# Optimization experiments

Measured on AMD Instinct MI355X. Metric: run time of the kernel, lower is better.

The kernel has to match this reference:

```python
import jax, jax.numpy as jnp
import numpy as np

N, E, IN_F, G, LATENT, HIDDEN, STEPS = 50000, 800000, 7, 16, 64, 128, 3
LN_EPS = 1e-6  # flax LayerNorm default


def setup_inputs() -> dict:
    key = jax.random.key(0)

    def rn(i, shape, scale=1.0):
        return jax.random.normal(jax.random.fold_in(key, i), shape, dtype=jnp.float32) * scale

    return {
        "nodes": rn(0, (N, IN_F)),
        "senders": jax.random.randint(jax.random.fold_in(key, 1), (E,), 0, N, dtype=jnp.int32),
        "receivers": jax.random.randint(jax.random.fold_in(key, 2), (E,), 0, N, dtype=jnp.int32),
        "g": rn(3, (G,)),
        "embed_w": rn(4, (IN_F, LATENT), IN_F ** -0.5),
        "embed_b": jnp.zeros((LATENT,), jnp.float32),
        "edge_w1_first": rn(5, (2 * LATENT + G, HIDDEN), (2 * LATENT + G) ** -0.5),
        "edge_w1_rest": rn(6, (STEPS - 1, 3 * LATENT + G, HIDDEN), (3 * LATENT + G) ** -0.5),
        "edge_b1": jnp.zeros((STEPS, HIDDEN), jnp.float32),
        "edge_w2": rn(7, (STEPS, HIDDEN, LATENT), HIDDEN ** -0.5),
        "edge_b2": jnp.zeros((STEPS, LATENT), jnp.float32),
        "node_w1": rn(8, (STEPS, 2 * LATENT + G, HIDDEN), (2 * LATENT + G) ** -0.5),
        "node_b1": jnp.zeros((STEPS, HIDDEN), jnp.float32),
        "node_w2": rn(9, (STEPS, HIDDEN, LATENT), HIDDEN ** -0.5),
        "node_b2": jnp.zeros((STEPS, LATENT), jnp.float32),
        "ln_scale": jnp.ones((STEPS, LATENT), jnp.float32),
        "ln_bias": jnp.zeros((STEPS, LATENT), jnp.float32),
        "dec_w": rn(10, (LATENT, IN_F), LATENT ** -0.5),
        "dec_b": jnp.zeros((IN_F,), jnp.float32),
    }


def _layer_norm(x, scale, bias):
    mu = jnp.mean(x, axis=-1, keepdims=True)
    var = jnp.var(x, axis=-1, keepdims=True)
    return (x - mu) * jax.lax.rsqrt(var + LN_EPS) * scale + bias


def reference(nodes, senders, receivers, g, embed_w, embed_b,
              edge_w1_first, edge_w1_rest, edge_b1, edge_w2, edge_b2,
              node_w1, node_b1, node_w2, node_b2, ln_scale, ln_bias,
              dec_w, dec_b):
    n_node = nodes.shape[0]
    n_edge = senders.shape[0]
    # node embedder (GraphMapFeatures with Dense(latent_size))
    h = nodes @ embed_w + embed_b                      # [N, LATENT]
    ge = jnp.broadcast_to(g[None, :], (n_edge, g.shape[0]))  # globals per edge
    gn = jnp.broadcast_to(g[None, :], (n_node, g.shape[0]))  # globals per node
    e = None
    for t in range(STEPS):
        s = h[senders]                                 # [E, LATENT] gather
        r = h[receivers]                               # [E, LATENT] gather
        if t == 0:
            # edges are None on the first step -> concat(senders, receivers, globals)
            e_in = jnp.concatenate([s, r, ge], axis=1)
            w1 = edge_w1_first
        else:
            e_in = jnp.concatenate([e, s, r, ge], axis=1)
            w1 = edge_w1_rest[t - 1]
        # edge MLP: Dense(hidden)+gelu, Dense(latent)
        e = jax.nn.gelu(e_in @ w1 + edge_b1[t]) @ edge_w2[t] + edge_b2[t]
        # aggregate messages at receivers (jraph default segment_sum)
        recv = jax.ops.segment_sum(e, receivers, num_segments=n_node)
        # node MLP on concat(nodes, received, globals)
        n_in = jnp.concatenate([h, recv, gn], axis=1)
        upd = jax.nn.gelu(n_in @ node_w1[t] + node_b1[t]) @ node_w2[t] + node_b2[t]
        h = h + upd                                    # skip connection on nodes
        h = _layer_norm(h, ln_scale[t], ln_bias[t])
    # node decoder back to in_features
    return h @ dec_w + dec_b
```

## Files before the change

kernel.cpp:

```cpp
#include <hip/hip_runtime.h>

#define NN 50000
#define NE 800000
#define INF 7
#define GD 16
#define LAT 64
#define HID 128

typedef unsigned short u16;
typedef __attribute__((ext_vector_type(8))) __bf16 bf16x8;
typedef __attribute__((ext_vector_type(4))) float f32x4;

__device__ __forceinline__ float bf2f(u16 u) {
  union { unsigned int i; float f; } v; v.i = ((unsigned int)u) << 16; return v.f;
}
__device__ __forceinline__ float blo(unsigned int u) {
  union { unsigned int i; float f; } v; v.i = u << 16; return v.f;
}
__device__ __forceinline__ float bhi(unsigned int u) {
  union { unsigned int i; float f; } v; v.i = u & 0xffff0000u; return v.f;
}
__device__ __forceinline__ u16 f2bf(float f) {
  union { float f; unsigned int i; } v; v.f = f;
  unsigned int x = v.i;
  return (u16)((x + 0x7fffu + ((x >> 16) & 1u)) >> 16);
}
__device__ __forceinline__ float gelu(float x) {
  float u = x * x;
  float p = fmaf(0.044715f * u, x, x);
  float e = __expf(-1.5957691216057308f * p);
  return x * __builtin_amdgcn_rcpf(e + 1.0f);
}

struct PackJobs {
  const float* src[13];
  u16* dst[13];
  int K[13];
  int N[13];
  int KC[13];
};

__global__ void pack_all(PackJobs J) {
  const int j = blockIdx.y;
  const int KC = J.KC[j];
  const float* W = J.src[j];
  u16* out = J.dst[j];
  int t = blockIdx.x * blockDim.x + threadIdx.x;
  if (KC == 0) {
    if (t < 32) out[t] = (t < GD) ? f2bf(W[t]) : (u16)0;
    return;
  }
  const int K = J.K[j], N = J.N[j];
  const int NT = N >> 4;
  if (t >= KC * NT * 64) return;
  int l = t & 63;
  int nt = (t >> 6) % NT;
  int kc = t / (64 * NT);
  int n = nt * 16 + (l & 15);
  int kbase = kc * 32 + (l >> 4) * 8;
  ushort4 lo, hi;
  u16 v[8];
#pragma unroll
  for (int jj = 0; jj < 8; ++jj) {
    int k = kbase + jj;
    v[jj] = (k < K) ? f2bf(W[k * N + n]) : (u16)0;
  }
  lo.x = v[0]; lo.y = v[1]; lo.z = v[2]; lo.w = v[3];
  hi.x = v[4]; hi.y = v[5]; hi.z = v[6]; hi.w = v[7];
  ushort4* dst = (ushort4*)&out[(size_t)t * 8];
  dst[0] = lo; dst[1] = hi;
}

__global__ void hist_kernel(const int* __restrict__ rcv, int* __restrict__ cnt) {
  int i = blockIdx.x * blockDim.x + threadIdx.x;
  if (i < NE) atomicAdd(&cnt[rcv[i]], 1);
}

__launch_bounds__(1024)
__global__ void scan_kernel(const int* __restrict__ cnt, int* __restrict__ rowptr,
                            int* __restrict__ cursor) {
  __shared__ int wsum[16];
  const int t = threadIdx.x;
  const int lane = t & 63;
  const int wid = t >> 6;
  int carry = 0;
  for (int base = 0; base < NN; base += 1024) {
    const int i = base + t;
    int v = (i < NN) ? cnt[i] : 0;
    int x = v;
#pragma unroll
    for (int off = 1; off < 64; off <<= 1) {
      int y = __shfl_up(x, off);
      if (lane >= off) x += y;
    }
    if (lane == 63) wsum[wid] = x;
    __syncthreads();
    if (wid == 0 && lane < 16) {
      int s = wsum[lane];
#pragma unroll
      for (int off = 1; off < 16; off <<= 1) {
        int y = __shfl_up(s, off);
        if (lane >= off) s += y;
      }
      wsum[lane] = s;
    }
    __syncthreads();
    const int excl = carry + (wid > 0 ? wsum[wid - 1] : 0) + (x - v);
    if (i < NN) { rowptr[i] = excl; cursor[i] = excl; }
    carry += wsum[15];
    __syncthreads();
  }
  if (t == 0) rowptr[NN] = NE;
}

__global__ void scatter_kernel(const int* __restrict__ snd, const int* __restrict__ rcv,
                               int* __restrict__ cursor, int* __restrict__ ssnd,
                               int* __restrict__ srcv) {
  int i = blockIdx.x * blockDim.x + threadIdx.x;
  if (i >= NE) return;
  int r = rcv[i];
  int p = atomicAdd(&cursor[r], 1);
  ssnd[p] = snd[i];
  srcv[p] = r;
}

__global__ void embed_kernel(const float* __restrict__ nodes, const float* __restrict__ w,
                             const float* __restrict__ b, float* __restrict__ h,
                             u16* __restrict__ hbf) {
  int gid = blockIdx.x * blockDim.x + threadIdx.x;
  if (gid >= NN * LAT) return;
  int n = gid >> 6, j = gid & 63;
  float acc = b[j];
#pragma unroll
  for (int k = 0; k < INF; ++k)
    acc = fmaf(nodes[n * INF + k], w[k * LAT + j], acc);
  h[gid] = acc;
  hbf[gid] = f2bf(acc);
}

__launch_bounds__(256)
__global__ void agg_kernel(const u16* __restrict__ ebuf, const int* __restrict__ rowptr,
                           u16* __restrict__ recvbf) {
  const int gid = blockIdx.x * blockDim.x + threadIdx.x;
  const int node = gid >> 6;
  if (node >= NN) return;
  const int lane = threadIdx.x & 63;
  const int sub = lane >> 3;
  const int c8 = (lane & 7) * 8;
  const int e0 = rowptr[node], e1 = rowptr[node + 1];
  float a[8] = {0.f, 0.f, 0.f, 0.f, 0.f, 0.f, 0.f, 0.f};
  for (int e = e0 + sub; e < e1; e += 8) {
    uint4 v = *(const uint4*)&ebuf[(size_t)e * 64 + c8];
    a[0] += blo(v.x); a[1] += bhi(v.x);
    a[2] += blo(v.y); a[3] += bhi(v.y);
    a[4] += blo(v.z); a[5] += bhi(v.z);
    a[6] += blo(v.w); a[7] += bhi(v.w);
  }
#pragma unroll
  for (int k = 0; k < 8; ++k) {
    a[k] += __shfl_xor(a[k], 8);
    a[k] += __shfl_xor(a[k], 16);
    a[k] += __shfl_xor(a[k], 32);
  }
  if (sub == 0) {
    ushort4 p0, p1;
    p0.x = f2bf(a[0]); p0.y = f2bf(a[1]); p0.z = f2bf(a[2]); p0.w = f2bf(a[3]);
    p1.x = f2bf(a[4]); p1.y = f2bf(a[5]); p1.z = f2bf(a[6]); p1.w = f2bf(a[7]);
    *(ushort4*)&recvbf[(size_t)node * 64 + c8]     = p0;
    *(ushort4*)&recvbf[(size_t)node * 64 + c8 + 4] = p1;
  }
}

template <int KC, bool FIRST>
__launch_bounds__(256, 2)
__global__ void edge_mfma(const u16* __restrict__ hbf, u16* __restrict__ ebuf,
                          const int* __restrict__ snd, const int* __restrict__ rcv,
                          const u16* __restrict__ gpad,
                          const u16* __restrict__ w1p, const float* __restrict__ b1,
                          const u16* __restrict__ w2p, const float* __restrict__ b2) {
  __shared__ __align__(16) u16 hid[32 * 136];
  __shared__ __align__(16) u16 easm[32 * 64];

  const int tid = threadIdx.x;
  const int lane = tid & 63;
  const int w = tid >> 6;
  const int l15 = lane & 15;
  const int q = lane >> 4;
  const int mr = w & 1;
  const int ntb1 = (w >> 1) * 4;
  const int ntb2 = (w >> 1) * 2;
  const int arow = mr * 16 + l15;
  const int NTILE = NE / 32;
  constexpr int AF = FIRST ? 4 : 6;

  float bb1[4], bb2[2];
#pragma unroll
  for (int i = 0; i < 4; ++i) bb1[i] = b1[(ntb1 + i) * 16 + l15];
#pragma unroll
  for (int i = 0; i < 2; ++i) bb2[i] = b2[(ntb2 + i) * 16 + l15];

  bf16x8 b1f[KC][4];
#pragma unroll
  for (int kc = 0; kc < KC; ++kc)
#pragma unroll
    for (int i = 0; i < 4; ++i)
      b1f[kc][i] = *(const bf16x8*)&w1p[(size_t)((kc * 8 + ntb1 + i) * 64 + lane) * 8];
  bf16x8 b2f[4][2];
#pragma unroll
  for (int kc = 0; kc < 4; ++kc)
#pragma unroll
    for (int i = 0; i < 2; ++i)
      b2f[kc][i] = *(const bf16x8*)&w2p[(size_t)((kc * 4 + ntb2 + i) * 64 + lane) * 8];
  const bf16x8 gfrag = *(const bf16x8*)&gpad[q * 8];

  bf16x8 acur[AF];
  int s_cur = 0, r_cur = 0;
  {
    const int t0 = blockIdx.x;
    if (t0 < NTILE) {
      const int eg0 = t0 * 32 + arow;
      const int s0 = snd[eg0], r0 = rcv[eg0];
      if (!FIRST) {
#pragma unroll
        for (int kc = 0; kc < 2; ++kc)
          acur[kc] = *(const bf16x8*)&ebuf[(size_t)eg0 * 64 + kc * 32 + q * 8];
      }
#pragma unroll
      for (int kc = 0; kc < 2; ++kc)
        acur[(FIRST ? 0 : 2) + kc] = *(const bf16x8*)&hbf[s0 * 64 + kc * 32 + q * 8];
#pragma unroll
      for (int kc = 0; kc < 2; ++kc)
        acur[(FIRST ? 2 : 4) + kc] = *(const bf16x8*)&hbf[r0 * 64 + kc * 32 + q * 8];
      const int t1 = t0 + gridDim.x;
      if (t1 < NTILE) {
        s_cur = snd[t1 * 32 + arow];
        r_cur = rcv[t1 * 32 + arow];
      }
    }
  }

  for (int tile = blockIdx.x; tile < NTILE; tile += gridDim.x) {
    const int ebase = tile * 32;

    f32x4 acc[4];
#pragma unroll
    for (int i = 0; i < 4; ++i) acc[i] = (f32x4){bb1[i], bb1[i], bb1[i], bb1[i]};
#pragma unroll
    for (int kc = 0; kc < KC; ++kc) {
      bf16x8 a = (kc < AF) ? acur[kc] : gfrag;
#pragma unroll
      for (int i = 0; i < 4; ++i)
        acc[i] = __builtin_amdgcn_mfma_f32_16x16x32_bf16(a, b1f[kc][i], acc[i], 0, 0, 0);
    }

    {
      const int tn = tile + gridDim.x;
      if (tn < NTILE) {
        const int egn = tn * 32 + arow;
        const int soffn = s_cur * 64;
        const int roffn = r_cur * 64;
        if (!FIRST) {
#pragma unroll
          for (int kc = 0; kc < 2; ++kc)
            acur[kc] = *(const bf16x8*)&ebuf[(size_t)egn * 64 + kc * 32 + q * 8];
        }
#pragma unroll
        for (int kc = 0; kc < 2; ++kc)
          acur[(FIRST ? 0 : 2) + kc] = *(const bf16x8*)&hbf[soffn + kc * 32 + q * 8];
#pragma unroll
        for (int kc = 0; kc < 2; ++kc)
          acur[(FIRST ? 2 : 4) + kc] = *(const bf16x8*)&hbf[roffn + kc * 32 + q * 8];
        const int tn2 = tn + gridDim.x;
        if (tn2 < NTILE) {
          s_cur = snd[tn2 * 32 + arow];
          r_cur = rcv[tn2 * 32 + arow];
        }
      }
    }

#pragma unroll
    for (int i = 0; i < 4; ++i) {
      const int col = (ntb1 + i) * 16 + l15;
#pragma unroll
      for (int r4 = 0; r4 < 4; ++r4) {
        const int row = mr * 16 + q * 4 + r4;
        hid[row * 136 + col] = f2bf(gelu(acc[i][r4]));
      }
    }
    asm volatile("s_waitcnt lgkmcnt(0)" ::: "memory");
    __builtin_amdgcn_s_barrier();

    {
      f32x4 acc2[2];
#pragma unroll
      for (int i = 0; i < 2; ++i) acc2[i] = (f32x4){bb2[i], bb2[i], bb2[i], bb2[i]};
#pragma unroll
      for (int kc = 0; kc < 4; ++kc) {
        bf16x8 a = *(const bf16x8*)&hid[arow * 136 + kc * 32 + q * 8];
#pragma unroll
        for (int i = 0; i < 2; ++i)
          acc2[i] = __builtin_amdgcn_mfma_f32_16x16x32_bf16(a, b2f[kc][i], acc2[i], 0, 0, 0);
      }
#pragma unroll
      for (int i = 0; i < 2; ++i) {
        const int col = (ntb2 + i) * 16 + l15;
#pragma unroll
        for (int r4 = 0; r4 < 4; ++r4) {
          const int row = mr * 16 + q * 4 + r4;
          easm[row * 64 + col] = f2bf(acc2[i][r4]);
        }
      }
    }
    asm volatile("s_waitcnt lgkmcnt(0)" ::: "memory");
    __builtin_amdgcn_s_barrier();
    ((uint4*)&ebuf[(size_t)ebase * 64])[tid] = ((const uint4*)easm)[tid];
  }
}

__launch_bounds__(256)
__global__ void node_mfma(float* __restrict__ h, u16* __restrict__ hbf,
                          const u16* __restrict__ recvbf,
                          const u16* __restrict__ gpad,
                          const u16* __restrict__ w1p, const float* __restrict__ b1,
                          const u16* __restrict__ w2p, const float* __restrict__ b2,
                          const float* __restrict__ lns, const float* __restrict__ lnb) {
  __shared__ __align__(16) u16 hid[32 * 136];
  __shared__ __align__(16) float outs[32 * 68];

  const int tid = threadIdx.x;
  const int lane = tid & 63;
  const int w = tid >> 6;
  const int l15 = lane & 15;
  const int q = lane >> 4;
  const int mr = w & 1;
  const int ntb1 = (w >> 1) * 4;
  const int ntb2 = (w >> 1) * 2;
  const int arow = mr * 16 + l15;

  float bb1[4], bb2[2];
#pragma unroll
  for (int i = 0; i < 4; ++i) bb1[i] = b1[(ntb1 + i) * 16 + l15];
#pragma unroll
  for (int i = 0; i < 2; ++i) bb2[i] = b2[(ntb2 + i) * 16 + l15];

  const int nrow = tid >> 3;
  const int jc = (tid & 7) * 8;
  float sc8[8], bi8[8];
#pragma unroll
  for (int k = 0; k < 8; ++k) { sc8[k] = lns[jc + k]; bi8[k] = lnb[jc + k]; }

  const int NT = (NN + 31) / 32;
  for (int tile = blockIdx.x; tile < NT; tile += gridDim.x) {
    const int nbase = tile * 32;
    const int na = min(nbase + arow, NN - 1) * 64;

    {
      f32x4 acc[4];
#pragma unroll
      for (int i = 0; i < 4; ++i) acc[i] = (f32x4){bb1[i], bb1[i], bb1[i], bb1[i]};
#pragma unroll
      for (int kc = 0; kc < 5; ++kc) {
        bf16x8 a;
        if (kc < 2) {
          a = *(const bf16x8*)&hbf[na + kc * 32 + q * 8];
        } else if (kc < 4) {
          a = *(const bf16x8*)&recvbf[na + (kc - 2) * 32 + q * 8];
        } else {
          a = *(const bf16x8*)&gpad[q * 8];
        }
#pragma unroll
        for (int i = 0; i < 4; ++i) {
          bf16x8 b = *(const bf16x8*)&w1p[(size_t)((kc * 8 + ntb1 + i) * 64 + lane) * 8];
          acc[i] = __builtin_amdgcn_mfma_f32_16x16x32_bf16(a, b, acc[i], 0, 0, 0);
        }
      }
#pragma unroll
      for (int i = 0; i < 4; ++i) {
        const int col = (ntb1 + i) * 16 + l15;
#pragma unroll
        for (int r4 = 0; r4 < 4; ++r4) {
          const int row = mr * 16 + q * 4 + r4;
          hid[row * 136 + col] = f2bf(gelu(acc[i][r4]));
        }
      }
    }
    __syncthreads();
    {
      f32x4 acc[2];
#pragma unroll
      for (int i = 0; i < 2; ++i) acc[i] = (f32x4){bb2[i], bb2[i], bb2[i], bb2[i]};
#pragma unroll
      for (int kc = 0; kc < 4; ++kc) {
        bf16x8 a = *(const bf16x8*)&hid[arow * 136 + kc * 32 + q * 8];
#pragma unroll
        for (int i = 0; i < 2; ++i) {
          bf16x8 b = *(const bf16x8*)&w2p[(size_t)((kc * 4 + ntb2 + i) * 64 + lane) * 8];
          acc[i] = __builtin_amdgcn_mfma_f32_16x16x32_bf16(a, b, acc[i], 0, 0, 0);
        }
      }
#pragma unroll
      for (int i = 0; i < 2; ++i) {
        const int col = (ntb2 + i) * 16 + l15;
#pragma unroll
        for (int r4 = 0; r4 < 4; ++r4) {
          const int row = mr * 16 + q * 4 + r4;
          outs[row * 68 + col] = acc[i][r4];
        }
      }
    }
    __syncthreads();
    {
      const int n = nbase + nrow;
      if (n < NN) {
        float x[8];
        float4 hv0 = *(const float4*)&h[n * 64 + jc];
        float4 hv1 = *(const float4*)&h[n * 64 + jc + 4];
        x[0] = hv0.x + outs[nrow * 68 + jc + 0];
        x[1] = hv0.y + outs[nrow * 68 + jc + 1];
        x[2] = hv0.z + outs[nrow * 68 + jc + 2];
        x[3] = hv0.w + outs[nrow * 68 + jc + 3];
        x[4] = hv1.x + outs[nrow * 68 + jc + 4];
        x[5] = hv1.y + outs[nrow * 68 + jc + 5];
        x[6] = hv1.z + outs[nrow * 68 + jc + 6];
        x[7] = hv1.w + outs[nrow * 68 + jc + 7];
        float s = 0.f, qq = 0.f;
#pragma unroll
        for (int k = 0; k < 8; ++k) { s += x[k]; qq += x[k] * x[k]; }
#pragma unroll
        for (int off = 1; off < 8; off <<= 1) {
          s += __shfl_xor(s, off);
          qq += __shfl_xor(qq, off);
        }
        float mean = s * (1.0f / 64.0f);
        float var = fmaxf(qq * (1.0f / 64.0f) - mean * mean, 0.0f);
        float rstd = rsqrtf(var + 1e-6f);
        float o[8];
        ushort4 ob0, ob1;
#pragma unroll
        for (int k = 0; k < 8; ++k) o[k] = (x[k] - mean) * rstd * sc8[k] + bi8[k];
        *(float4*)&h[n * 64 + jc]     = make_float4(o[0], o[1], o[2], o[3]);
        *(float4*)&h[n * 64 + jc + 4] = make_float4(o[4], o[5], o[6], o[7]);
        ob0.x = f2bf(o[0]); ob0.y = f2bf(o[1]); ob0.z = f2bf(o[2]); ob0.w = f2bf(o[3]);
        ob1.x = f2bf(o[4]); ob1.y = f2bf(o[5]); ob1.z = f2bf(o[6]); ob1.w = f2bf(o[7]);
        *(ushort4*)&hbf[n * 64 + jc]     = ob0;
        *(ushort4*)&hbf[n * 64 + jc + 4] = ob1;
      }
    }
    __syncthreads();
  }
}

__global__ void decode_kernel(const float* __restrict__ h, const float* __restrict__ w,
                              const float* __restrict__ b, float* __restrict__ out) {
  int gid = blockIdx.x * blockDim.x + threadIdx.x;
  if (gid >= NN * INF) return;
  int n = gid / 7, f = gid % 7;
  float acc = b[f];
#pragma unroll
  for (int k = 0; k < LAT; ++k)
    acc = fmaf(h[n * 64 + k], w[k * 7 + f], acc);
  out[gid] = acc;
}

extern "C" void kernel_launch(void* const* d_in, const int* in_sizes, int n_in,
                              void* d_out, int out_size, void* d_ws, size_t ws_size,
                              hipStream_t stream) {
  const float* nodes = (const float*)d_in[0];
  const int* senders = (const int*)d_in[1];
  const int* recvrs  = (const int*)d_in[2];
  const float* g     = (const float*)d_in[3];
  const float* emb_w = (const float*)d_in[4];
  const float* emb_b = (const float*)d_in[5];
  const float* ew1f  = (const float*)d_in[6];
  const float* ew1r  = (const float*)d_in[7];
  const float* eb1   = (const float*)d_in[8];
  const float* ew2   = (const float*)d_in[9];
  const float* eb2   = (const float*)d_in[10];
  const float* nw1   = (const float*)d_in[11];
  const float* nb1   = (const float*)d_in[12];
  const float* nw2   = (const float*)d_in[13];
  const float* nb2   = (const float*)d_in[14];
  const float* lns   = (const float*)d_in[15];
  const float* lnb   = (const float*)d_in[16];
  const float* dw    = (const float*)d_in[17];
  const float* db    = (const float*)d_in[18];

  char* cur = (char*)d_ws;
  float* h      = (float*)cur;  cur += (size_t)NN * LAT * 4;
  u16*   ebuf   = (u16*)cur;    cur += (size_t)NE * LAT * 2;
  u16*   hbf    = (u16*)cur;    cur += (size_t)NN * LAT * 2;
  u16*   recvbf = (u16*)cur;    cur += (size_t)NN * LAT * 2;
  u16*   ew1p[3]; for (int t = 0; t < 3; ++t) { ew1p[t] = (u16*)cur; cur += 7 * 8 * 64 * 8 * 2; }
  u16*   ew2p[3]; for (int t = 0; t < 3; ++t) { ew2p[t] = (u16*)cur; cur += 4 * 4 * 64 * 8 * 2; }
  u16*   nw1p[3]; for (int t = 0; t < 3; ++t) { nw1p[t] = (u16*)cur; cur += 5 * 8 * 64 * 8 * 2; }
  u16*   nw2p[3]; for (int t = 0; t < 3; ++t) { nw2p[t] = (u16*)cur; cur += 4 * 4 * 64 * 8 * 2; }
  u16*   gpad   = (u16*)cur;    cur += 256;
  int*   cnt    = (int*)cur;    cur += ((size_t)NN * 4 + 255) & ~(size_t)255;
  int*   cursor = (int*)cur;    cur += ((size_t)NN * 4 + 255) & ~(size_t)255;
  int*   rowptr = (int*)cur;    cur += ((size_t)(NN + 1) * 4 + 255) & ~(size_t)255;
  int*   ssnd   = (int*)cur;    cur += (size_t)NE * 4;
  int*   srcv   = (int*)cur;    cur += (size_t)NE * 4;

  hipMemsetAsync(cnt, 0, (size_t)NN * 4, stream);
  hist_kernel<<<(NE + 255) / 256, 256, 0, stream>>>(recvrs, cnt);
  scan_kernel<<<1, 1024, 0, stream>>>(cnt, rowptr, cursor);
  scatter_kernel<<<(NE + 255) / 256, 256, 0, stream>>>(senders, recvrs, cursor, ssnd, srcv);

  PackJobs J;
  J.src[0] = ew1f;                       J.dst[0] = ew1p[0]; J.K[0] = 144; J.N[0] = 128; J.KC[0] = 5;
  J.src[1] = ew1r;                       J.dst[1] = ew1p[1]; J.K[1] = 208; J.N[1] = 128; J.KC[1] = 7;
  J.src[2] = ew1r + (size_t)208 * 128;   J.dst[2] = ew1p[2]; J.K[2] = 208; J.N[2] = 128; J.KC[2] = 7;
  for (int t = 0; t < 3; ++t) {
    J.src[3 + t] = ew2 + (size_t)t * 128 * 64;  J.dst[3 + t] = ew2p[t]; J.K[3 + t] = 128; J.N[3 + t] = 64; J.KC[3 + t] = 4;
    J.src[6 + t] = nw1 + (size_t)t * 144 * 128; J.dst[6 + t] = nw1p[t]; J.K[6 + t] = 144; J.N[6 + t] = 128; J.KC[6 + t] = 5;
    J.src[9 + t] = nw2 + (size_t)t * 128 * 64;  J.dst[9 + t] = nw2p[t]; J.K[9 + t] = 128; J.N[9 + t] = 64; J.KC[9 + t] = 4;
  }
  J.src[12] = g; J.dst[12] = gpad; J.K[12] = 0; J.N[12] = 0; J.KC[12] = 0;
  pack_all<<<dim3(16, 13), 256, 0, stream>>>(J);

  embed_kernel<<<(NN * LAT + 255) / 256, 256, 0, stream>>>(nodes, emb_w, emb_b, h, hbf);

  for (int t = 0; t < 3; ++t) {
    if (t == 0)
      edge_mfma<5, true><<<2048, 256, 0, stream>>>(hbf, ebuf,
          ssnd, srcv, gpad, ew1p[0], eb1, ew2p[0], eb2);
    else
      edge_mfma<7, false><<<2048, 256, 0, stream>>>(hbf, ebuf,
          ssnd, srcv, gpad, ew1p[t], eb1 + t * 128, ew2p[t], eb2 + t * 64);
    agg_kernel<<<(NN * 64 + 255) / 256, 256, 0, stream>>>(ebuf, rowptr, recvbf);
    node_mfma<<<1563, 256, 0, stream>>>(h, hbf, recvbf, gpad,
        nw1p[t], nb1 + t * 128, nw2p[t], nb2 + t * 64,
        lns + t * 64, lnb + t * 64);
  }

  decode_kernel<<<(NN * INF + 255) / 256, 256, 0, stream>>>(h, dw, db, (float*)d_out);
}
```

Measured before the change: 629.8 us.

## Widen edge MLP tile to 64 edges and stream weights instead of register-caching

The edge kernel now processes 64 edges per tile, with each wave covering all four 16-row subtiles and a slice of output columns. Weight fragments are no longer held in registers for the kernel's lifetime; they are reloaded from global/L2 per k-chunk and reused across four row tiles. This frees registers, doubles gather prefetch depth and raises work per barrier, but adds repeated weight loads and larger shared buffers (easm is padded to 72 columns). The grid size changes from 2048 to 2084 blocks.

```diff
diff --git a/kernel.cpp b/kernel.cpp
--- a/kernel.cpp
+++ b/kernel.cpp
@@ -178,142 +178,152 @@
                           const u16* __restrict__ gpad,
                           const u16* __restrict__ w1p, const float* __restrict__ b1,
                           const u16* __restrict__ w2p, const float* __restrict__ b2) {
-  __shared__ __align__(16) u16 hid[32 * 136];
-  __shared__ __align__(16) u16 easm[32 * 64];
+  __shared__ __align__(16) u16 hid[64 * 136];
+  __shared__ __align__(16) u16 easm[64 * 72];
 
   const int tid = threadIdx.x;
   const int lane = tid & 63;
   const int w = tid >> 6;
   const int l15 = lane & 15;
   const int q = lane >> 4;
-  const int mr = w & 1;
-  const int ntb1 = (w >> 1) * 4;
-  const int ntb2 = (w >> 1) * 2;
-  const int arow = mr * 16 + l15;
-  const int NTILE = NE / 32;
+  const int NTILE = NE / 64;
   constexpr int AF = FIRST ? 4 : 6;
 
-  float bb1[4], bb2[2];
-#pragma unroll
-  for (int i = 0; i < 4; ++i) bb1[i] = b1[(ntb1 + i) * 16 + l15];
-#pragma unroll
-  for (int i = 0; i < 2; ++i) bb2[i] = b2[(ntb2 + i) * 16 + l15];
-
-  bf16x8 b1f[KC][4];
-#pragma unroll
-  for (int kc = 0; kc < KC; ++kc)
-#pragma unroll
-    for (int i = 0; i < 4; ++i)
-      b1f[kc][i] = *(const bf16x8*)&w1p[(size_t)((kc * 8 + ntb1 + i) * 64 + lane) * 8];
-  bf16x8 b2f[4][2];
-#pragma unroll
-  for (int kc = 0; kc < 4; ++kc)
-#pragma unroll
-    for (int i = 0; i < 2; ++i)
-      b2f[kc][i] = *(const bf16x8*)&w2p[(size_t)((kc * 4 + ntb2 + i) * 64 + lane) * 8];
+  float bb1[2];
+  bb1[0] = b1[(2 * w) * 16 + l15];
+  bb1[1] = b1[(2 * w + 1) * 16 + l15];
+  const float bb2 = b2[w * 16 + l15];
   const bf16x8 gfrag = *(const bf16x8*)&gpad[q * 8];
 
-  bf16x8 acur[AF];
-  int s_cur = 0, r_cur = 0;
+  bf16x8 acur[4][AF];
+  int s_cur[4], r_cur[4];
   {
     const int t0 = blockIdx.x;
     if (t0 < NTILE) {
-      const int eg0 = t0 * 32 + arow;
-      const int s0 = snd[eg0], r0 = rcv[eg0];
-      if (!FIRST) {
+#pragma unroll
+      for (int rt = 0; rt < 4; ++rt) {
+        const int eg0 = t0 * 64 + rt * 16 + l15;
+        const int s0 = snd[eg0], r0 = rcv[eg0];
+        if (!FIRST) {
+#pragma unroll
+          for (int kc = 0; kc < 2; ++kc)
+            acur[rt][kc] = *(const bf16x8*)&ebuf[(size_t)eg0 * 64 + kc * 32 + q * 8];
+        }
 #pragma unroll
         for (int kc = 0; kc < 2; ++kc)
-          acur[kc] = *(const bf16x8*)&ebuf[(size_t)eg0 * 64 + kc * 32 + q * 8];
-      }
-#pragma unroll
-      for (int kc = 0; kc < 2; ++kc)
-        acur[(FIRST ? 0 : 2) + kc] = *(const bf16x8*)&hbf[s0 * 64 + kc * 32 + q * 8];
-#pragma unroll
-      for (int kc = 0; kc < 2; ++kc)
-        acur[(FIRST ? 2 : 4) + kc] = *(const bf16x8*)&hbf[r0 * 64 + kc * 32 + q * 8];
+          acur[rt][(FIRST ? 0 : 2) + kc] = *(const bf16x8*)&hbf[s0 * 64 + kc * 32 + q * 8];
+#pragma unroll
+        for (int kc = 0; kc < 2; ++kc)
+          acur[rt][(FIRST ? 2 : 4) + kc] = *(const bf16x8*)&hbf[r0 * 64 + kc * 32 + q * 8];
+      }
       const int t1 = t0 + gridDim.x;
       if (t1 < NTILE) {
-        s_cur = snd[t1 * 32 + arow];
-        r_cur = rcv[t1 * 32 + arow];
+#pragma unroll
+        for (int rt = 0; rt < 4; ++rt) {
+          s_cur[rt] = snd[t1 * 64 + rt * 16 + l15];
+          r_cur[rt] = rcv[t1 * 64 + rt * 16 + l15];
+        }
       }
     }
   }
 
   for (int tile = blockIdx.x; tile < NTILE; tile += gridDim.x) {
-    const int ebase = tile * 32;
-
-    f32x4 acc[4];
-#pragma unroll
-    for (int i = 0; i < 4; ++i) acc[i] = (f32x4){bb1[i], bb1[i], bb1[i], bb1[i]};
+    const int ebase = tile * 64;
+
+    f32x4 acc[4][2];
+#pragma unroll
+    for (int rt = 0; rt < 4; ++rt)
+#pragma unroll
+      for (int i = 0; i < 2; ++i)
+        acc[rt][i] = (f32x4){bb1[i], bb1[i], bb1[i], bb1[i]};
 #pragma unroll
     for (int kc = 0; kc < KC; ++kc) {
-      bf16x8 a = (kc < AF) ? acur[kc] : gfrag;
-#pragma unroll
-      for (int i = 0; i < 4; ++i)
-        acc[i] = __builtin_amdgcn_mfma_f32_16x16x32_bf16(a, b1f[kc][i], acc[i], 0, 0, 0);
+      bf16x8 bw0 = *(const bf16x8*)&w1p[(size_t)((kc * 8 + 2 * w) * 64 + lane) * 8];
+      bf16x8 bw1 = *(const bf16x8*)&w1p[(size_t)((kc * 8 + 2 * w + 1) * 64 + lane) * 8];
+#pragma unroll
+      for (int rt = 0; rt < 4; ++rt) {
+        bf16x8 a = (kc < AF) ? acur[rt][kc] : gfrag;
+        acc[rt][0] = __builtin_amdgcn_mfma_f32_16x16x32_bf16(a, bw0, acc[rt][0], 0, 0, 0);
+        acc[rt][1] = __builtin_amdgcn_mfma_f32_16x16x32_bf16(a, bw1, acc[rt][1], 0, 0, 0);
+      }
     }
 
     {
       const int tn = tile + gridDim.x;
       if (tn < NTILE) {
-        const int egn = tn * 32 + arow;
-        const int soffn = s_cur * 64;
-        const int roffn = r_cur * 64;
-        if (!FIRST) {
+#pragma unroll
+        for (int rt = 0; rt < 4; ++rt) {
+          const int egn = tn * 64 + rt * 16 + l15;
+          const int soffn = s_cur[rt] * 64;
+          const int roffn = r_cur[rt] * 64;
+          if (!FIRST) {
+#pragma unroll
+            for (int kc = 0; kc < 2; ++kc)
+              acur[rt][kc] = *(const bf16x8*)&ebuf[(size_t)egn * 64 + kc * 32 + q * 8];
+          }
 #pragma unroll
           for (int kc = 0; kc < 2; ++kc)
-            acur[kc] = *(const bf16x8*)&ebuf[(size_t)egn * 64 + kc * 32 + q * 8];
-        }
-#pragma unroll
-        for (int kc = 0; kc < 2; ++kc)
-          acur[(FIRST ? 0 : 2) + kc] = *(const bf16x8*)&hbf[soffn + kc * 32 + q * 8];
-#pragma unroll
-        for (int kc = 0; kc < 2; ++kc)
-          acur[(FIRST ? 2 : 4) + kc] = *(const bf16x8*)&hbf[roffn + kc * 32 + q * 8];
+            acur[rt][(FIRST ? 0 : 2) + kc] = *(const bf16x8*)&hbf[soffn + kc * 32 + q * 8];
+#pragma unroll
+          for (int kc = 0; kc < 2; ++kc)
+            acur[rt][(FIRST ? 2 : 4) + kc] = *(const bf16x8*)&hbf[roffn + kc * 32 + q * 8];
+        }
         const int tn2 = tn + gridDim.x;
         if (tn2 < NTILE) {
-          s_cur = snd[tn2 * 32 + arow];
-          r_cur = rcv[tn2 * 32 + arow];
-        }
-      }
-    }
-
-#pragma unroll
-    for (int i = 0; i < 4; ++i) {
-      const int col = (ntb1 + i) * 16 + l15;
-#pragma unroll
-      for (int r4 = 0; r4 < 4; ++r4) {
-        const int row = mr * 16 + q * 4 + r4;
-        hid[row * 136 + col] = f2bf(gelu(acc[i][r4]));
-      }
-    }
+#pragma unroll
+          for (int rt = 0; rt < 4; ++rt) {
+            s_cur[rt] = snd[tn2 * 64 + rt * 16 + l15];
+            r_cur[rt] = rcv[tn2 * 64 + rt * 16 + l15];
+          }
+        }
+      }
+    }
+
+#pragma unroll
+    for (int rt = 0; rt < 4; ++rt)
+#pragma unroll
+      for (int i = 0; i < 2; ++i) {
+        const int col = (2 * w + i) * 16 + l15;
+#pragma unroll
+        for (int r4 = 0; r4 < 4; ++r4) {
+          const int row = rt * 16 + q * 4 + r4;
+          hid[row * 136 + col] = f2bf(gelu(acc[rt][i][r4]));
+        }
+      }
     asm volatile("s_waitcnt lgkmcnt(0)" ::: "memory");
     __builtin_amdgcn_s_barrier();
 
     {
-      f32x4 acc2[2];
-#pragma unroll
-      for (int i = 0; i < 2; ++i) acc2[i] = (f32x4){bb2[i], bb2[i], bb2[i], bb2[i]};
+      f32x4 acc2[4];
+#pragma unroll
+      for (int rt = 0; rt < 4; ++rt) acc2[rt] = (f32x4){bb2, bb2, bb2, bb2};
 #pragma unroll
       for (int kc = 0; kc < 4; ++kc) {
-        bf16x8 a = *(const bf16x8*)&hid[arow * 136 + kc * 32 + q * 8];
-#pragma unroll
-        for (int i = 0; i < 2; ++i)
-          acc2[i] = __builtin_amdgcn_mfma_f32_16x16x32_bf16(a, b2f[kc][i], acc2[i], 0, 0, 0);
-      }
-#pragma unroll
-      for (int i = 0; i < 2; ++i) {
-        const int col = (ntb2 + i) * 16 + l15;
+        bf16x8 bw = *(const bf16x8*)&w2p[(size_t)((kc * 4 + w) * 64 + lane) * 8];
+#pragma unroll
+        for (int rt = 0; rt < 4; ++rt) {
+          bf16x8 a = *(const bf16x8*)&hid[(rt * 16 + l15) * 136 + kc * 32 + q * 8];
+          acc2[rt] = __builtin_amdgcn_mfma_f32_16x16x32_bf16(a, bw, acc2[rt], 0, 0, 0);
+        }
+      }
+#pragma unroll
+      for (int rt = 0; rt < 4; ++rt) {
+        const int col = w * 16 + l15;
 #pragma unroll
         for (int r4 = 0; r4 < 4; ++r4) {
-          const int row = mr * 16 + q * 4 + r4;
-          easm[row * 64 + col] = f2bf(acc2[i][r4]);
+          const int row = rt * 16 + q * 4 + r4;
+          easm[row * 72 + col] = f2bf(acc2[rt][r4]);
         }
       }
     }
     asm volatile("s_waitcnt lgkmcnt(0)" ::: "memory");
     __builtin_amdgcn_s_barrier();
-    ((uint4*)&ebuf[(size_t)ebase * 64])[tid] = ((const uint4*)easm)[tid];
+#pragma unroll
+    for (int part = 0; part < 2; ++part) {
+      const int idx = part * 256 + tid;
+      const int r = idx >> 3, c = (idx & 7) * 8;
+      ((uint4*)&ebuf[(size_t)ebase * 64])[idx] = *(const uint4*)&easm[r * 72 + c];
+    }
   }
 }
 
@@ -522,10 +532,10 @@
 
   for (int t = 0; t < 3; ++t) {
     if (t == 0)
-      edge_mfma<5, true><<<2048, 256, 0, stream>>>(hbf, ebuf,
+      edge_mfma<5, true><<<2084, 256, 0, stream>>>(hbf, ebuf,
           ssnd, srcv, gpad, ew1p[0], eb1, ew2p[0], eb2);
     else
-      edge_mfma<7, false><<<2048, 256, 0, stream>>>(hbf, ebuf,
+      edge_mfma<7, false><<<2084, 256, 0, stream>>>(hbf, ebuf,
           ssnd, srcv, gpad, ew1p[t], eb1 + t * 128, ew2p[t], eb2 + t * 64);
     agg_kernel<<<(NN * 64 + 255) / 256, 256, 0, stream>>>(ebuf, rowptr, recvbf);
     node_mfma<<<1563, 256, 0, stream>>>(h, hbf, recvbf, gpad,
```

After: 803.5 us. 1.28x slower.
